# Performance work log

Measured on AMD Instinct MI355X. Metric: run time of the kernel, lower is better.

## Reference

```python
import jax, jax.numpy as jnp
import numpy as np

N = 50000
E = 800000
IN_C, HID, OUT_C = 128, 128, 64
EPS = 1e-5


def gcn_conv(x, edge_index, W, b):
    # x: [N, F_in], edge_index: [2, E], W: [F_in, F_out], b: [F_out]
    src, dst = edge_index[0], edge_index[1]
    h = x @ W  # [N, F_out]
    # degree with self-loops (edge weight 1)
    deg = 1.0 + jax.ops.segment_sum(jnp.ones((E,), h.dtype), dst, num_segments=N)
    dinv = jax.lax.rsqrt(deg)  # deg^{-1/2}
    coef = dinv[src] * dinv[dst]  # [E]
    msg = h[src] * coef[:, None]  # gather + scale
    agg = jax.ops.segment_sum(msg, dst, num_segments=N)
    agg = agg + h * (dinv * dinv)[:, None]  # self-loop term deg^{-1}
    return agg + b


def bn_eval(x, gamma, beta, mean, var):
    return (x - mean) * jax.lax.rsqrt(var + EPS) * gamma + beta


def leaky(x):
    return jnp.where(x > 0, x, 0.1 * x)


def setup_inputs() -> dict:
    key = jax.random.key(0)
    ks = jax.random.split(key, 12)
    x = jax.random.normal(ks[0], (N, IN_C), jnp.float32)
    edge_index = jax.random.randint(ks[1], (2, E), 0, N, dtype=jnp.int64)
    s1 = 1.0 / np.sqrt(IN_C)
    s2 = 1.0 / np.sqrt(HID)
    W1 = jax.random.uniform(ks[2], (IN_C, HID), jnp.float32, -s1, s1)
    b1 = jnp.zeros((HID,), jnp.float32)
    W2 = jax.random.uniform(ks[3], (HID, HID), jnp.float32, -s2, s2)
    b2 = jnp.zeros((HID,), jnp.float32)
    W3 = jax.random.uniform(ks[4], (HID, OUT_C), jnp.float32, -s2, s2)
    b3 = jnp.zeros((OUT_C,), jnp.float32)
    g1 = jnp.ones((HID,), jnp.float32)
    be1 = jnp.zeros((HID,), jnp.float32)
    m1 = 0.1 * jax.random.normal(ks[5], (HID,), jnp.float32)
    v1 = jax.random.uniform(ks[6], (HID,), jnp.float32, 0.5, 1.5)
    g2 = jnp.ones((HID,), jnp.float32)
    be2 = jnp.zeros((HID,), jnp.float32)
    m2 = 0.1 * jax.random.normal(ks[7], (HID,), jnp.float32)
    v2 = jax.random.uniform(ks[8], (HID,), jnp.float32, 0.5, 1.5)
    return dict(x=x, edge_index=edge_index, W1=W1, b1=b1, g1=g1, be1=be1, m1=m1, v1=v1,
                W2=W2, b2=b2, g2=g2, be2=be2, m2=m2, v2=v2, W3=W3, b3=b3)


def reference(x, edge_index, W1, b1, g1, be1, m1, v1, W2, b2, g2, be2, m2, v2, W3, b3):
    h = gcn_conv(x, edge_index, W1, b1)
    h = leaky(bn_eval(h, g1, be1, m1, v1))
    # dropout is identity at inference
    h = gcn_conv(h, edge_index, W2, b2)
    h = leaky(bn_eval(h, g2, be2, m2, v2))
    z = gcn_conv(h, edge_index, W3, b3)
    return z
```

## Files before the change

kernel.cpp:

```cpp
#include <hip/hip_runtime.h>
#include <hip/hip_fp16.h>


#define LRELU_SLOPE 0.1f
#define BN_EPS 1e-5f

typedef _Float16 half8 __attribute__((ext_vector_type(8)));
typedef float f32x4 __attribute__((ext_vector_type(4)));

__global__ void zero_i32(int* __restrict__ p, int n) {
    int i = blockIdx.x * blockDim.x + threadIdx.x;
    if (i < n) p[i] = 0;
}

__global__ void hist_kernel(const int* __restrict__ dst, int* __restrict__ cnt, int E) {
    int i = blockIdx.x * blockDim.x + threadIdx.x;
    if (i < E) atomicAdd(&cnt[dst[i]], 1);
}

__global__ void prep_w(const float* __restrict__ W1, const float* __restrict__ W2,
                       const float* __restrict__ W3, _Float16* __restrict__ W1t,
                       _Float16* __restrict__ W2t, _Float16* __restrict__ W3t) {
    int i = blockIdx.x * 256 + threadIdx.x;
    if (i < 16384) {
        int k = i >> 7, c = i & 127;
        W1t[c * 136 + k] = (_Float16)W1[i];
    } else if (i < 32768) {
        int j = i - 16384;
        int k = j >> 7, c = j & 127;
        W2t[c * 136 + k] = (_Float16)W2[j];
    } else if (i < 40960) {
        int j = i - 32768;
        int k = j >> 6, c = j & 63;
        W3t[c * 136 + k] = (_Float16)W3[j];
    }
}

__global__ void scan1(const int* __restrict__ cnt, int* __restrict__ incl,
                      int* __restrict__ part, int n) {
    __shared__ int s[256];
    int tid = threadIdx.x;
    int gid = blockIdx.x * 256 + tid;
    int v = (gid < n) ? cnt[gid] : 0;
    s[tid] = v;
    __syncthreads();
    for (int off = 1; off < 256; off <<= 1) {
        int t = (tid >= off) ? s[tid - off] : 0;
        __syncthreads();
        s[tid] += t;
        __syncthreads();
    }
    if (gid < n) incl[gid] = s[tid];
    if (tid == 255) part[blockIdx.x] = s[255];
}

__global__ void scan2(const int* __restrict__ part, int* __restrict__ poff, int nb) {
    __shared__ int s[256];
    int tid = threadIdx.x;
    int v = (tid < nb) ? part[tid] : 0;
    s[tid] = v;
    __syncthreads();
    for (int off = 1; off < 256; off <<= 1) {
        int t = (tid >= off) ? s[tid - off] : 0;
        __syncthreads();
        s[tid] += t;
        __syncthreads();
    }
    poff[tid] = s[tid] - v;
}

__global__ void scan3(const int* __restrict__ cnt, const int* __restrict__ incl,
                      const int* __restrict__ poff, int* __restrict__ row_ptr,
                      int* __restrict__ cursor, float* __restrict__ dinv, int n, int E) {
    int gid = blockIdx.x * 256 + threadIdx.x;
    if (gid < n) {
        int c = cnt[gid];
        int rp = incl[gid] - c + poff[blockIdx.x];
        row_ptr[gid] = rp;
        cursor[gid] = rp;
        dinv[gid] = rsqrtf(1.0f + (float)c);
    }
    if (gid == 0) row_ptr[n] = E;
}

__global__ void scatter_kernel(const int* __restrict__ src, const int* __restrict__ dst,
                               int* __restrict__ cursor, int* __restrict__ ssrc, int E) {
    int i = blockIdx.x * blockDim.x + threadIdx.x;
    if (i < E) {
        int d = dst[i];
        int pos = atomicAdd(&cursor[d], 1);
        ssrc[pos] = src[i];
    }
}

template <int NC, bool AF32>
__global__ __launch_bounds__(256) void gemm_mfma(const void* __restrict__ Ain,
                                                 const _Float16* __restrict__ Wt,
                                                 const float* __restrict__ dinv,
                                                 __half* __restrict__ H, int nrows) {
    constexpr int NT = NC / 16;
    constexpr int SPH = (NC == 128) ? 136 : 88;
    __shared__ _Float16 smem[NC * 136];

    const int tid = threadIdx.x;
    const int row0 = blockIdx.x * 64;

    {
        const uint4* src = reinterpret_cast<const uint4*>(Wt);
        uint4* dst = reinterpret_cast<uint4*>(smem);
        for (int i = tid; i < NC * 17; i += 256) dst[i] = src[i];
    }
    __syncthreads();

    const int w = tid >> 6;
    const int lane = tid & 63;
    const int l15 = lane & 15;
    const int kg = lane >> 4;

    int ar = row0 + w * 16 + l15;
    if (ar > nrows - 1) ar = nrows - 1;
    half8 a[4];
#pragma unroll
    for (int ks = 0; ks < 4; ++ks) {
        const int cb = ks * 32 + kg * 8;
        if constexpr (AF32) {
            const float* Xf = (const float*)Ain;
            const float4 x0 = *reinterpret_cast<const float4*>(&Xf[(size_t)ar * 128 + cb]);
            const float4 x1 = *reinterpret_cast<const float4*>(&Xf[(size_t)ar * 128 + cb + 4]);
            half8 av;
            av[0] = (_Float16)x0.x; av[1] = (_Float16)x0.y;
            av[2] = (_Float16)x0.z; av[3] = (_Float16)x0.w;
            av[4] = (_Float16)x1.x; av[5] = (_Float16)x1.y;
            av[6] = (_Float16)x1.z; av[7] = (_Float16)x1.w;
            a[ks] = av;
        } else {
            const __half* Xh = (const __half*)Ain;
            a[ks] = *reinterpret_cast<const half8*>(&Xh[(size_t)ar * 128 + cb]);
        }
    }

    f32x4 acc[NT];
#pragma unroll
    for (int nt = 0; nt < NT; ++nt) acc[nt] = {0.f, 0.f, 0.f, 0.f};

#pragma unroll
    for (int nt = 0; nt < NT; ++nt) {
        const int c = nt * 16 + l15;
#pragma unroll
        for (int ks = 0; ks < 4; ++ks) {
            const half8 b = *reinterpret_cast<const half8*>(&smem[c * 136 + ks * 32 + kg * 8]);
            acc[nt] = __builtin_amdgcn_mfma_f32_16x16x32_f16(a[ks], b, acc[nt], 0, 0, 0);
        }
    }

    __syncthreads();

    float dv[4];
#pragma unroll
    for (int r = 0; r < 4; ++r) {
        int gr = row0 + w * 16 + kg * 4 + r;
        if (gr > nrows - 1) gr = nrows - 1;
        dv[r] = dinv[gr];
    }
    _Float16* Hl = smem;
#pragma unroll
    for (int nt = 0; nt < NT; ++nt) {
#pragma unroll
        for (int r = 0; r < 4; ++r) {
            Hl[(w * 16 + kg * 4 + r) * SPH + nt * 16 + l15] = (_Float16)(acc[nt][r] * dv[r]);
        }
    }
    __syncthreads();

    constexpr int CG = NC / 8;
    for (int i = tid; i < 64 * CG; i += 256) {
        const int row = i / CG, cg = i % CG;
        const int gr = row0 + row;
        if (gr < nrows) {
            *reinterpret_cast<uint4*>(&H[(size_t)gr * NC + cg * 8]) =
                *reinterpret_cast<const uint4*>(&Hl[row * SPH + cg * 8]);
        }
    }
}

__device__ __forceinline__ float2 u2f2(unsigned u) {
    __half2 h;
    *reinterpret_cast<unsigned*>(&h) = u;
    return __half22float2(h);
}

template <int NC, bool BN, bool HOUT>
__global__ __launch_bounds__(256) void agg_h(
    const __half* __restrict__ H, const int* __restrict__ row_ptr,
    const int* __restrict__ ssrc, const float* __restrict__ dinv,
    const float* __restrict__ b, const float* __restrict__ g,
    const float* __restrict__ be, const float* __restrict__ m,
    const float* __restrict__ v, void* __restrict__ out, int n) {
    constexpr int FPT = NC / 32;
    const int tid = threadIdx.x;
    const int node = blockIdx.x * 8 + (tid >> 5);
    const int lane = tid & 31;
    const int f0 = lane * FPT;
    if (node >= n) return;

    const int e0 = row_ptr[node];
    const int e1 = row_ptr[node + 1];

    if constexpr (FPT == 4) {
        uint2 su = *reinterpret_cast<const uint2*>(&H[(size_t)node * NC + f0]);
        float2 slo = u2f2(su.x), shi = u2f2(su.y);
        float4 A0 = {slo.x, slo.y, shi.x, shi.y};
        float4 A1 = {0, 0, 0, 0}, A2 = {0, 0, 0, 0}, A3 = {0, 0, 0, 0};
        int e = e0;
        for (; e + 3 < e1; e += 4) {
            const int sA = ssrc[e], sB = ssrc[e + 1], sC = ssrc[e + 2], sD = ssrc[e + 3];
            const uint2 uA = *reinterpret_cast<const uint2*>(&H[(size_t)sA * NC + f0]);
            const uint2 uB = *reinterpret_cast<const uint2*>(&H[(size_t)sB * NC + f0]);
            const uint2 uC = *reinterpret_cast<const uint2*>(&H[(size_t)sC * NC + f0]);
            const uint2 uD = *reinterpret_cast<const uint2*>(&H[(size_t)sD * NC + f0]);
            float2 l, h;
            l = u2f2(uA.x); h = u2f2(uA.y);
            A0.x += l.x; A0.y += l.y; A0.z += h.x; A0.w += h.y;
            l = u2f2(uB.x); h = u2f2(uB.y);
            A1.x += l.x; A1.y += l.y; A1.z += h.x; A1.w += h.y;
            l = u2f2(uC.x); h = u2f2(uC.y);
            A2.x += l.x; A2.y += l.y; A2.z += h.x; A2.w += h.y;
            l = u2f2(uD.x); h = u2f2(uD.y);
            A3.x += l.x; A3.y += l.y; A3.z += h.x; A3.w += h.y;
        }
        for (; e < e1; ++e) {
            const uint2 u = *reinterpret_cast<const uint2*>(&H[(size_t)ssrc[e] * NC + f0]);
            float2 l = u2f2(u.x), h = u2f2(u.y);
            A1.x += l.x; A1.y += l.y; A1.z += h.x; A1.w += h.y;
        }
        float4 acc;
        acc.x = (A0.x + A1.x) + (A2.x + A3.x);
        acc.y = (A0.y + A1.y) + (A2.y + A3.y);
        acc.z = (A0.z + A1.z) + (A2.z + A3.z);
        acc.w = (A0.w + A1.w) + (A2.w + A3.w);
        const float dn = dinv[node];
        float o[4] = {acc.x * dn + b[f0], acc.y * dn + b[f0 + 1],
                      acc.z * dn + b[f0 + 2], acc.w * dn + b[f0 + 3]};
        if constexpr (BN) {
#pragma unroll
            for (int j = 0; j < 4; ++j) {
                float val = (o[j] - m[f0 + j]) * rsqrtf(v[f0 + j] + BN_EPS) * g[f0 + j] + be[f0 + j];
                o[j] = val > 0.f ? val : LRELU_SLOPE * val;
            }
        }
        if constexpr (HOUT) {
            __half2 p0 = __floats2half2_rn(o[0], o[1]);
            __half2 p1 = __floats2half2_rn(o[2], o[3]);
            uint2 st;
            st.x = *reinterpret_cast<unsigned*>(&p0);
            st.y = *reinterpret_cast<unsigned*>(&p1);
            *reinterpret_cast<uint2*>(&((__half*)out)[(size_t)node * NC + f0]) = st;
        } else {
            float4 ov = {o[0], o[1], o[2], o[3]};
            *reinterpret_cast<float4*>(&((float*)out)[(size_t)node * NC + f0]) = ov;
        }
    } else {
        unsigned su = *reinterpret_cast<const unsigned*>(&H[(size_t)node * NC + f0]);
        float2 A0 = u2f2(su);
        float2 A1 = {0, 0}, A2 = {0, 0}, A3 = {0, 0};
        int e = e0;
        for (; e + 3 < e1; e += 4) {
            const int sA = ssrc[e], sB = ssrc[e + 1], sC = ssrc[e + 2], sD = ssrc[e + 3];
            const unsigned uA = *reinterpret_cast<const unsigned*>(&H[(size_t)sA * NC + f0]);
            const unsigned uB = *reinterpret_cast<const unsigned*>(&H[(size_t)sB * NC + f0]);
            const unsigned uC = *reinterpret_cast<const unsigned*>(&H[(size_t)sC * NC + f0]);
            const unsigned uD = *reinterpret_cast<const unsigned*>(&H[(size_t)sD * NC + f0]);
            float2 f;
            f = u2f2(uA); A0.x += f.x; A0.y += f.y;
            f = u2f2(uB); A1.x += f.x; A1.y += f.y;
            f = u2f2(uC); A2.x += f.x; A2.y += f.y;
            f = u2f2(uD); A3.x += f.x; A3.y += f.y;
        }
        for (; e < e1; ++e) {
            float2 f = u2f2(*reinterpret_cast<const unsigned*>(&H[(size_t)ssrc[e] * NC + f0]));
            A1.x += f.x; A1.y += f.y;
        }
        float2 acc;
        acc.x = (A0.x + A1.x) + (A2.x + A3.x);
        acc.y = (A0.y + A1.y) + (A2.y + A3.y);
        const float dn = dinv[node];
        float o0 = acc.x * dn + b[f0];
        float o1 = acc.y * dn + b[f0 + 1];
        if constexpr (BN) {
            o0 = (o0 - m[f0]) * rsqrtf(v[f0] + BN_EPS) * g[f0] + be[f0];
            o0 = o0 > 0.f ? o0 : LRELU_SLOPE * o0;
            o1 = (o1 - m[f0 + 1]) * rsqrtf(v[f0 + 1] + BN_EPS) * g[f0 + 1] + be[f0 + 1];
            o1 = o1 > 0.f ? o1 : LRELU_SLOPE * o1;
        }
        if constexpr (HOUT) {
            __half2 p0 = __floats2half2_rn(o0, o1);
            *reinterpret_cast<unsigned*>(&((__half*)out)[(size_t)node * NC + f0]) =
                *reinterpret_cast<unsigned*>(&p0);
        } else {
            float2 ov = {o0, o1};
            *reinterpret_cast<float2*>(&((float*)out)[(size_t)node * NC + f0]) = ov;
        }
    }
}

extern "C" void kernel_launch(void* const* d_in, const int* in_sizes, int n_in,
                              void* d_out, int out_size, void* d_ws, size_t ws_size,
                              hipStream_t stream) {
    const float* x  = (const float*)d_in[0];
    const int* ei   = (const int*)d_in[1];
    const float* W1 = (const float*)d_in[2];
    const float* b1 = (const float*)d_in[3];
    const float* g1 = (const float*)d_in[4];
    const float* be1= (const float*)d_in[5];
    const float* m1 = (const float*)d_in[6];
    const float* v1 = (const float*)d_in[7];
    const float* W2 = (const float*)d_in[8];
    const float* b2 = (const float*)d_in[9];
    const float* g2 = (const float*)d_in[10];
    const float* be2= (const float*)d_in[11];
    const float* m2 = (const float*)d_in[12];
    const float* v2 = (const float*)d_in[13];
    const float* W3 = (const float*)d_in[14];
    const float* b3 = (const float*)d_in[15];
    float* out = (float*)d_out;

    const int N = in_sizes[0] / 128;
    const int E = in_sizes[1] / 2;
    const int* srcIdx = ei;
    const int* dstIdx = ei + E;

    char* p = (char*)d_ws;
    auto carve = [&](size_t bytes) -> void* {
        void* r = (void*)p;
        p += (bytes + 255) & ~(size_t)255;
        return r;
    };
    int* cnt       = (int*)carve((size_t)N * 4);
    int* incl      = (int*)carve((size_t)N * 4);
    int* part      = (int*)carve(1024);
    int* poff      = (int*)carve(1024);
    int* row_ptr   = (int*)carve((size_t)(N + 1) * 4);
    int* cursor    = (int*)carve((size_t)N * 4);
    float* dinv    = (float*)carve((size_t)N * 4);
    int* ssrc      = (int*)carve((size_t)E * 4);
    __half* Hb     = (__half*)carve((size_t)N * 128 * 2);
    __half* Xb     = (__half*)carve((size_t)N * 128 * 2);
    _Float16* W1t  = (_Float16*)carve(128 * 136 * 2);
    _Float16* W2t  = (_Float16*)carve(128 * 136 * 2);
    _Float16* W3t  = (_Float16*)carve(64 * 136 * 2);
    (void)ws_size; (void)n_in; (void)out_size;

    const int nb_n = (N + 255) / 256;
    const int nb_e = (E + 255) / 256;

    prep_w<<<160, 256, 0, stream>>>(W1, W2, W3, W1t, W2t, W3t);
    zero_i32<<<nb_n, 256, 0, stream>>>(cnt, N);
    hist_kernel<<<nb_e, 256, 0, stream>>>(dstIdx, cnt, E);
    scan1<<<nb_n, 256, 0, stream>>>(cnt, incl, part, N);
    scan2<<<1, 256, 0, stream>>>(part, poff, nb_n);
    scan3<<<nb_n, 256, 0, stream>>>(cnt, incl, poff, row_ptr, cursor, dinv, N, E);
    scatter_kernel<<<nb_e, 256, 0, stream>>>(srcIdx, dstIdx, cursor, ssrc, E);

    const int gb = (N + 63) / 64;
    const int ab = (N + 7) / 8;

    gemm_mfma<128, true><<<gb, 256, 0, stream>>>(x, W1t, dinv, Hb, N);
    agg_h<128, true, true><<<ab, 256, 0, stream>>>(
        Hb, row_ptr, ssrc, dinv, b1, g1, be1, m1, v1, Xb, N);

    gemm_mfma<128, false><<<gb, 256, 0, stream>>>(Xb, W2t, dinv, Hb, N);
    agg_h<128, true, true><<<ab, 256, 0, stream>>>(
        Hb, row_ptr, ssrc, dinv, b2, g2, be2, m2, v2, Xb, N);

    gemm_mfma<64, false><<<gb, 256, 0, stream>>>(Xb, W3t, dinv, Hb, N);
    agg_h<64, false, false><<<ab, 256, 0, stream>>>(
        Hb, row_ptr, ssrc, dinv, b3, nullptr, nullptr, nullptr, nullptr, out, N);
}
```

Baseline: 310.8 us.

## Build CSR via two-level bucket binning with shared-memory atomics

Replaces the global-atomic histogram and scatter with a bucketed approach. Edges are first binned by dst>>10 into 64 fixed-capacity buckets using block-local shared counters. Per-bucket histograms and CSR fills then run with shared-memory atomics. This cuts contended global atomics and random scatters, at the cost of an extra pairs buffer and a fixed BCAP per bucket that could overflow on skewed inputs. bin_pass also uses a 3200-entry shared buffer, which assumes E/256 <= 3200.

```diff
diff --git a/kernel.cpp b/kernel.cpp
--- a/kernel.cpp
+++ b/kernel.cpp
@@ -4,18 +4,126 @@
 
 #define LRELU_SLOPE 0.1f
 #define BN_EPS 1e-5f
+#define BCAP 20480
 
 typedef _Float16 half8 __attribute__((ext_vector_type(8)));
 typedef float f32x4 __attribute__((ext_vector_type(4)));
 
-__global__ void zero_i32(int* __restrict__ p, int n) {
-    int i = blockIdx.x * blockDim.x + threadIdx.x;
-    if (i < n) p[i] = 0;
-}
-
-__global__ void hist_kernel(const int* __restrict__ dst, int* __restrict__ cnt, int E) {
-    int i = blockIdx.x * blockDim.x + threadIdx.x;
-    if (i < E) atomicAdd(&cnt[dst[i]], 1);
+__global__ void init_bcur(int* __restrict__ bcur) {
+    int i = threadIdx.x;
+    if (i < 64) bcur[i] = i * BCAP;
+}
+
+__global__ __launch_bounds__(256) void bin_pass(const int* __restrict__ src,
+                                                const int* __restrict__ dst, int E,
+                                                int* __restrict__ bcur,
+                                                unsigned long long* __restrict__ pairs) {
+    __shared__ int sd[3200], ss[3200];
+    __shared__ int lcur[64];
+    const int tid = threadIdx.x;
+    const int chunk = (E + gridDim.x - 1) / gridDim.x;
+    const int e0 = blockIdx.x * chunk;
+    const int ecnt = min(chunk, E - e0);
+    for (int j = tid; j < ecnt; j += 256) {
+        sd[j] = dst[e0 + j];
+        ss[j] = src[e0 + j];
+    }
+    if (tid < 64) lcur[tid] = 0;
+    __syncthreads();
+    for (int j = tid; j < ecnt; j += 256) atomicAdd(&lcur[sd[j] >> 10], 1);
+    __syncthreads();
+    if (tid < 64) lcur[tid] = atomicAdd(&bcur[tid], lcur[tid]);
+    __syncthreads();
+    for (int j = tid; j < ecnt; j += 256) {
+        const int b = sd[j] >> 10;
+        const int pos = atomicAdd(&lcur[b], 1);
+        pairs[pos] = ((unsigned long long)(unsigned)ss[j] << 32) | (unsigned)sd[j];
+    }
+}
+
+__global__ __launch_bounds__(512) void hist_bucket(const unsigned long long* __restrict__ pairs,
+                                                   const int* __restrict__ bcur,
+                                                   int* __restrict__ cnt, int N) {
+    __shared__ int h[1024];
+    const int b = blockIdx.x;
+    const int base = b << 10;
+    const int nn = min(1024, N - base);
+    const int cntb = bcur[b] - b * BCAP;
+    for (int i = threadIdx.x; i < 1024; i += 512) h[i] = 0;
+    __syncthreads();
+    const unsigned long long* pb = pairs + (size_t)b * BCAP;
+    for (int j = threadIdx.x; j < cntb; j += 512) {
+        const int d = (int)(pb[j] & 0xffffffffull);
+        atomicAdd(&h[d - base], 1);
+    }
+    __syncthreads();
+    for (int i = threadIdx.x; i < nn; i += 512) cnt[base + i] = h[i];
+}
+
+__global__ void scan1(const int* __restrict__ cnt, int* __restrict__ incl,
+                      int* __restrict__ part, int n) {
+    __shared__ int s[256];
+    int tid = threadIdx.x;
+    int gid = blockIdx.x * 256 + tid;
+    int v = (gid < n) ? cnt[gid] : 0;
+    s[tid] = v;
+    __syncthreads();
+    for (int off = 1; off < 256; off <<= 1) {
+        int t = (tid >= off) ? s[tid - off] : 0;
+        __syncthreads();
+        s[tid] += t;
+        __syncthreads();
+    }
+    if (gid < n) incl[gid] = s[tid];
+    if (tid == 255) part[blockIdx.x] = s[255];
+}
+
+__global__ void scan2(const int* __restrict__ part, int* __restrict__ poff, int nb) {
+    __shared__ int s[256];
+    int tid = threadIdx.x;
+    int v = (tid < nb) ? part[tid] : 0;
+    s[tid] = v;
+    __syncthreads();
+    for (int off = 1; off < 256; off <<= 1) {
+        int t = (tid >= off) ? s[tid - off] : 0;
+        __syncthreads();
+        s[tid] += t;
+        __syncthreads();
+    }
+    poff[tid] = s[tid] - v;
+}
+
+__global__ void scan3(const int* __restrict__ cnt, const int* __restrict__ incl,
+                      const int* __restrict__ poff, int* __restrict__ row_ptr,
+                      float* __restrict__ dinv, int n, int E) {
+    int gid = blockIdx.x * 256 + threadIdx.x;
+    if (gid < n) {
+        int c = cnt[gid];
+        row_ptr[gid] = incl[gid] - c + poff[blockIdx.x];
+        dinv[gid] = rsqrtf(1.0f + (float)c);
+    }
+    if (gid == 0) row_ptr[n] = E;
+}
+
+__global__ __launch_bounds__(512) void build_csr(const unsigned long long* __restrict__ pairs,
+                                                 const int* __restrict__ bcur,
+                                                 const int* __restrict__ row_ptr,
+                                                 int* __restrict__ ssrc_g, int N) {
+    __shared__ int cur[1024];
+    const int b = blockIdx.x;
+    const int base = b << 10;
+    const int nn = min(1024, N - base);
+    const int cntb = bcur[b] - b * BCAP;
+    for (int i = threadIdx.x; i < nn; i += 512) cur[i] = row_ptr[base + i];
+    __syncthreads();
+    const unsigned long long* pb = pairs + (size_t)b * BCAP;
+    for (int j = threadIdx.x; j < cntb; j += 512) {
+        const unsigned long long p = pb[j];
+        const int d = (int)(p & 0xffffffffull);
+        const int s = (int)(p >> 32);
+        const int pos = atomicAdd(&cur[d - base], 1);
+        ssrc_g[pos] = s;
+    }
 }
 
 __global__ void prep_w(const float* __restrict__ W1, const float* __restrict__ W2,
@@ -33,63 +141,6 @@
         int j = i - 32768;
         int k = j >> 6, c = j & 63;
         W3t[c * 136 + k] = (_Float16)W3[j];
-    }
-}
-
-__global__ void scan1(const int* __restrict__ cnt, int* __restrict__ incl,
-                      int* __restrict__ part, int n) {
-    __shared__ int s[256];
-    int tid = threadIdx.x;
-    int gid = blockIdx.x * 256 + tid;
-    int v = (gid < n) ? cnt[gid] : 0;
-    s[tid] = v;
-    __syncthreads();
-    for (int off = 1; off < 256; off <<= 1) {
-        int t = (tid >= off) ? s[tid - off] : 0;
-        __syncthreads();
-        s[tid] += t;
-        __syncthreads();
-    }
-    if (gid < n) incl[gid] = s[tid];
-    if (tid == 255) part[blockIdx.x] = s[255];
-}
-
-__global__ void scan2(const int* __restrict__ part, int* __restrict__ poff, int nb) {
-    __shared__ int s[256];
-    int tid = threadIdx.x;
-    int v = (tid < nb) ? part[tid] : 0;
-    s[tid] = v;
-    __syncthreads();
-    for (int off = 1; off < 256; off <<= 1) {
-        int t = (tid >= off) ? s[tid - off] : 0;
-        __syncthreads();
-        s[tid] += t;
-        __syncthreads();
-    }
-    poff[tid] = s[tid] - v;
-}
-
-__global__ void scan3(const int* __restrict__ cnt, const int* __restrict__ incl,
-                      const int* __restrict__ poff, int* __restrict__ row_ptr,
-                      int* __restrict__ cursor, float* __restrict__ dinv, int n, int E) {
-    int gid = blockIdx.x * 256 + threadIdx.x;
-    if (gid < n) {
-        int c = cnt[gid];
-        int rp = incl[gid] - c + poff[blockIdx.x];
-        row_ptr[gid] = rp;
-        cursor[gid] = rp;
-        dinv[gid] = rsqrtf(1.0f + (float)c);
-    }
-    if (gid == 0) row_ptr[n] = E;
-}
-
-__global__ void scatter_kernel(const int* __restrict__ src, const int* __restrict__ dst,
-                               int* __restrict__ cursor, int* __restrict__ ssrc, int E) {
-    int i = blockIdx.x * blockDim.x + threadIdx.x;
-    if (i < E) {
-        int d = dst[i];
-        int pos = atomicAdd(&cursor[d], 1);
-        ssrc[pos] = src[i];
     }
 }
 
@@ -328,6 +379,7 @@
     const int E = in_sizes[1] / 2;
     const int* srcIdx = ei;
     const int* dstIdx = ei + E;
+    const int nbuck = (N + 1023) >> 10;
 
     char* p = (char*)d_ws;
     auto carve = [&](size_t bytes) -> void* {
@@ -340,9 +392,10 @@
     int* part      = (int*)carve(1024);
     int* poff      = (int*)carve(1024);
     int* row_ptr   = (int*)carve((size_t)(N + 1) * 4);
-    int* cursor    = (int*)carve((size_t)N * 4);
+    int* bcur      = (int*)carve(64 * 4);
     float* dinv    = (float*)carve((size_t)N * 4);
     int* ssrc      = (int*)carve((size_t)E * 4);
+    unsigned long long* pairs = (unsigned long long*)carve((size_t)nbuck * BCAP * 8);
     __half* Hb     = (__half*)carve((size_t)N * 128 * 2);
     __half* Xb     = (__half*)carve((size_t)N * 128 * 2);
     _Float16* W1t  = (_Float16*)carve(128 * 136 * 2);
@@ -351,15 +404,15 @@
     (void)ws_size; (void)n_in; (void)out_size;
 
     const int nb_n = (N + 255) / 256;
-    const int nb_e = (E + 255) / 256;
 
     prep_w<<<160, 256, 0, stream>>>(W1, W2, W3, W1t, W2t, W3t);
-    zero_i32<<<nb_n, 256, 0, stream>>>(cnt, N);
-    hist_kernel<<<nb_e, 256, 0, stream>>>(dstIdx, cnt, E);
+    init_bcur<<<1, 64, 0, stream>>>(bcur);
+    bin_pass<<<256, 256, 0, stream>>>(srcIdx, dstIdx, E, bcur, pairs);
+    hist_bucket<<<nbuck, 512, 0, stream>>>(pairs, bcur, cnt, N);
     scan1<<<nb_n, 256, 0, stream>>>(cnt, incl, part, N);
     scan2<<<1, 256, 0, stream>>>(part, poff, nb_n);
-    scan3<<<nb_n, 256, 0, stream>>>(cnt, incl, poff, row_ptr, cursor, dinv, N, E);
-    scatter_kernel<<<nb_e, 256, 0, stream>>>(srcIdx, dstIdx, cursor, ssrc, E);
+    scan3<<<nb_n, 256, 0, stream>>>(cnt, incl, poff, row_ptr, dinv, N, E);
+    build_csr<<<nbuck, 512, 0, stream>>>(pairs, bcur, row_ptr, ssrc, N);
 
     const int gb = (N + 63) / 64;
     const int ab = (N + 7) / 8;
```

Result: faster. 266.1 us (-14.4%).
